# Kernel tuning notes

Hardware: AMD Instinct MI355X
Metric: run time of the kernel (lower is better)

Reference implementation:

```python
import jax, jax.numpy as jnp
import numpy as np
import math

H, KV, D, HID, WIN = 8, 4, 256, 2048, 1024  # heads, kv heads, head_dim, hidden, sliding window
B, S = 1, 2048

def _rms(x, scale):
    # Gemma3RMSNorm: hardcoded 1e-6 eps, (1+scale) gain
    var = jnp.mean(jnp.square(x), axis=-1, keepdims=True)
    return x * jax.lax.rsqrt(var + 1e-6) * (1.0 + scale)

def _rot_half(x):
    x1, x2 = jnp.split(x, 2, axis=-1)
    return jnp.concatenate((-x2, x1), axis=-1)

def setup_inputs() -> dict:
    key = jax.random.key(0)
    ks = jax.random.split(key, 8)
    x = jax.random.normal(ks[0], (B, S, HID), jnp.float32)
    attn_mask = jnp.ones((B, S), jnp.bool_)
    segment_pos = jnp.broadcast_to(jnp.arange(S, dtype=jnp.int32)[None], (B, S))
    # true RoPE tables, theta=1e6 (Gemma3 global layers)
    inv_freq = 1.0 / (1e6 ** (np.arange(0, D, 2, dtype=np.float32) / D))
    ang = np.arange(S, dtype=np.float32)[:, None] * inv_freq[None, :]  # [S, D/2]
    emb = np.concatenate([ang, ang], axis=-1)                          # [S, D]
    cos = jnp.asarray(np.cos(emb), jnp.float32)[None]                  # [1, S, D]
    sin = jnp.asarray(np.sin(emb), jnp.float32)[None]
    sd = 1.0 / math.sqrt(HID)
    wq = jax.random.normal(ks[1], (HID, H * D), jnp.float32) * sd
    wk = jax.random.normal(ks[2], (HID, KV * D), jnp.float32) * sd
    wv = jax.random.normal(ks[3], (HID, KV * D), jnp.float32) * sd
    wo = jax.random.normal(ks[4], (H * D, HID), jnp.float32) * (1.0 / math.sqrt(H * D))
    q_scale = jnp.zeros((D,), jnp.float32)  # zeros_init as in module
    k_scale = jnp.zeros((D,), jnp.float32)
    return dict(x=x, attn_mask=attn_mask, segment_pos=segment_pos, cos=cos, sin=sin,
                wq=wq, wk=wk, wv=wv, wo=wo, q_scale=q_scale, k_scale=k_scale)

def reference(x, attn_mask, segment_pos, cos, sin, wq, wk, wv, wo, q_scale, k_scale):
    b, s, _ = x.shape
    # projections -> [b, h, s, d]
    q = (x @ wq).reshape(b, s, H, D).transpose(0, 2, 1, 3)
    k = (x @ wk).reshape(b, s, KV, D).transpose(0, 2, 1, 3)
    v = (x @ wv).reshape(b, s, KV, D).transpose(0, 2, 1, 3)
    # per-head QK RMSNorm
    q = _rms(q, q_scale)
    k = _rms(k, k_scale)
    # RoPE (cos/sin broadcast over head axis, unsqueeze_dim=1)
    c, sn = cos[:, None], sin[:, None]
    q = q * c + _rot_half(q) * sn
    k = k * c + _rot_half(k) * sn
    # GQA: repeat-interleave kv heads
    rep = H // KV
    k = jnp.repeat(k, rep, axis=1)
    v = jnp.repeat(v, rep, axis=1)
    scores = jnp.einsum('bhqd,bhkd->bhqk', q, k) / math.sqrt(D)
    # causal + padding mask (q_len > 1 path, no image bidirectional mask)
    causal = jnp.tril(jnp.ones((s, s), jnp.bool_))
    mask = causal[None] & attn_mask[:, None, :]          # [b, q, kv]
    # sliding window mask (prefill: cache positions = arange)
    kvpos = jnp.arange(s)
    pos = segment_pos[:, :, None]
    sliding = (kvpos[None, None] > pos - WIN) & (kvpos[None, None] < pos + WIN)
    full = mask & sliding
    scores = scores + jnp.where(full[:, None], 0.0, -1e37)
    w = jax.nn.softmax(scores.astype(jnp.float32), axis=-1).astype(scores.dtype)
    out = jnp.einsum('bhqk,bhkd->bhqd', w, v)
    out = out.transpose(0, 2, 1, 3).reshape(b, s, H * D)
    return out @ wo
```

## Files before the change

### kernel.cpp

```cpp
#include <hip/hip_runtime.h>
#include <hip/hip_bf16.h>

#define S_LEN 2048
#define HID 2048
#define NH 8
#define NKV 4
#define HD 256
#define WIN 1024

typedef __hip_bfloat16 bf16;
typedef __attribute__((ext_vector_type(8))) short bf16x8;
typedef __attribute__((ext_vector_type(4))) float f32x4;

__device__ __forceinline__ void gld_lds16(void* lds, const void* g) {
    __builtin_amdgcn_global_load_lds(
        (const __attribute__((address_space(1))) unsigned int*)g,
        (__attribute__((address_space(3))) unsigned int*)lds,
        16, 0, 0);
}


__global__ __launch_bounds__(256)
void conv_f32_bf16(const float* __restrict__ s, bf16* __restrict__ d, int n8) {
    const int i = blockIdx.x * 256 + threadIdx.x;
    if (i >= n8) return;
    float4 a = ((const float4*)s)[i * 2];
    float4 b = ((const float4*)s)[i * 2 + 1];
    union { uint4 v; bf16 h[8]; } u;
    u.h[0] = __float2bfloat16(a.x); u.h[1] = __float2bfloat16(a.y);
    u.h[2] = __float2bfloat16(a.z); u.h[3] = __float2bfloat16(a.w);
    u.h[4] = __float2bfloat16(b.x); u.h[5] = __float2bfloat16(b.y);
    u.h[6] = __float2bfloat16(b.z); u.h[7] = __float2bfloat16(b.w);
    ((uint4*)d)[i] = u.v;
}

__global__ __launch_bounds__(256)
void convT_f32_bf16(const float* __restrict__ src, bf16* __restrict__ dst, int R, int C) {
    __shared__ bf16 Ts[64][72];
    const int tid = threadIdx.x;
    const int r0 = blockIdx.y * 64, c0 = blockIdx.x * 64;
    {
        const int r = tid >> 2;
        const int cq = (tid & 3) * 16;
#pragma unroll
        for (int j = 0; j < 16; j += 4) {
            float4 v = *(const float4*)&src[(size_t)(r0 + r) * C + c0 + cq + j];
            Ts[cq + j + 0][r] = __float2bfloat16(v.x);
            Ts[cq + j + 1][r] = __float2bfloat16(v.y);
            Ts[cq + j + 2][r] = __float2bfloat16(v.z);
            Ts[cq + j + 3][r] = __float2bfloat16(v.w);
        }
    }
    __syncthreads();
    {
        const int c = tid >> 2;
        const int rq = (tid & 3) * 16;
#pragma unroll
        for (int j = 0; j < 16; j += 8)
            *(uint4*)&dst[(size_t)(c0 + c) * R + r0 + rq + j] = *(const uint4*)&Ts[c][rq + j];
    }
}

template<int MODE>
__global__ __launch_bounds__(256)
void gemm_mfma2(const bf16* __restrict__ A, const bf16* __restrict__ Bt,
                float* __restrict__ C, bf16* __restrict__ Qo,
                bf16* __restrict__ Ko, bf16* __restrict__ Vto,
                int N, int K) {
    __shared__ bf16 As[128][32];
    __shared__ bf16 Bs[64][32];
    const int tid = threadIdx.x;
    const int w = tid >> 6, lane = tid & 63;
    const int lnm = lane & 15, quad = lane >> 4;
    const int wm = (w & 1) * 64, wn = (w >> 1) * 32;
    const int m0 = blockIdx.y * 128, n0 = blockIdx.x * 64;

    const int lr = lane >> 2;
    const int lc = (lane & 3) * 8;

    f32x4 acc[4][2];
#pragma unroll
    for (int i = 0; i < 4; ++i)
#pragma unroll
        for (int j = 0; j < 2; ++j) acc[i][j] = (f32x4){0.f, 0.f, 0.f, 0.f};

    const bf16* a0 = A + (size_t)(m0 + 32 * w + lr) * K + lc;
    const bf16* a1 = A + (size_t)(m0 + 32 * w + 16 + lr) * K + lc;
    const bf16* b0 = Bt + (size_t)(n0 + 16 * w + lr) * K + lc;

    for (int k0 = 0; k0 < K; k0 += 32) {
        gld_lds16(&As[32 * w][0],      a0 + k0);
        gld_lds16(&As[32 * w + 16][0], a1 + k0);
        gld_lds16(&Bs[16 * w][0],      b0 + k0);
        __syncthreads();
        bf16x8 af[4], bfr[2];
#pragma unroll
        for (int t = 0; t < 4; ++t) af[t] = *(const bf16x8*)&As[wm + t * 16 + lnm][quad * 8];
#pragma unroll
        for (int t = 0; t < 2; ++t) bfr[t] = *(const bf16x8*)&Bs[wn + t * 16 + lnm][quad * 8];
#pragma unroll
        for (int tm = 0; tm < 4; ++tm)
#pragma unroll
            for (int tn = 0; tn < 2; ++tn)
                acc[tm][tn] = __builtin_amdgcn_mfma_f32_16x16x32_bf16(
                    af[tm], bfr[tn], acc[tm][tn], 0, 0, 0);
        __syncthreads();
    }

#pragma unroll
    for (int tm = 0; tm < 4; ++tm)
#pragma unroll
        for (int tn = 0; tn < 2; ++tn)
#pragma unroll
            for (int r = 0; r < 4; ++r) {
                const int row = m0 + wm + tm * 16 + quad * 4 + r;
                const int col = n0 + wn + tn * 16 + lnm;
                const float v = acc[tm][tn][r];
                if constexpr (MODE == 0) {
                    C[(size_t)row * N + col] = v;
                } else {
                    if (col < 2048)
                        Qo[(size_t)row * (NH * HD) + col] = __float2bfloat16(v);
                    else if (col < 3072)
                        Ko[(size_t)row * (NKV * HD) + col - 2048] = __float2bfloat16(v);
                    else
                        Vto[(size_t)(col - 3072) * S_LEN + row] = __float2bfloat16(v);
                }
            }
}

__global__ __launch_bounds__(64)
void rmsrope_kernel(bf16* __restrict__ Q, bf16* __restrict__ Kb,
                    const float* __restrict__ cosb, const float* __restrict__ sinb,
                    const float* __restrict__ qscale, const float* __restrict__ kscale,
                    float qmul) {
    const int p = blockIdx.x;
    const int hg = blockIdx.y;
    const int lane = threadIdx.x;

    bf16* base;
    const float* scale;
    float mul;
    if (hg < NH) { base = Q + (size_t)p * (NH * HD) + hg * HD; scale = qscale; mul = qmul; }
    else         { base = Kb + (size_t)p * (NKV * HD) + (hg - NH) * HD; scale = kscale; mul = 1.f; }

    const int d0 = lane * 2;
    float x0 = (float)base[d0],       x1 = (float)base[d0 + 1];
    float y0 = (float)base[d0 + 128], y1 = (float)base[d0 + 129];

    float ss = x0 * x0 + x1 * x1 + y0 * y0 + y1 * y1;
#pragma unroll
    for (int off = 32; off > 0; off >>= 1) ss += __shfl_xor(ss, off, 64);
    const float r = rsqrtf(ss * (1.0f / (float)HD) + 1e-6f);

    x0 *= r * (1.f + scale[d0]);
    x1 *= r * (1.f + scale[d0 + 1]);
    y0 *= r * (1.f + scale[d0 + 128]);
    y1 *= r * (1.f + scale[d0 + 129]);

    const size_t cb = (size_t)p * HD;
    const float c0 = cosb[cb + d0],       c1 = cosb[cb + d0 + 1];
    const float cA = cosb[cb + d0 + 128], cB = cosb[cb + d0 + 129];
    const float s0 = sinb[cb + d0],       s1 = sinb[cb + d0 + 1];
    const float sA = sinb[cb + d0 + 128], sB = sinb[cb + d0 + 129];

    base[d0]       = __float2bfloat16((x0 * c0 - y0 * s0) * mul);
    base[d0 + 1]   = __float2bfloat16((x1 * c1 - y1 * s1) * mul);
    base[d0 + 128] = __float2bfloat16((y0 * cA + x0 * sA) * mul);
    base[d0 + 129] = __float2bfloat16((y1 * cB + x1 * sB) * mul);
}

__global__ __launch_bounds__(256)
void attn_mfma(const bf16* __restrict__ Q, const bf16* __restrict__ K,
               const bf16* __restrict__ Vt, bf16* __restrict__ Op,
               float2* __restrict__ ml) {
    __shared__ bf16 Ks[32][264];
    __shared__ bf16 Vs[256][40];
    __shared__ bf16 Pl[4][16][40];
    const int qt = blockIdx.x, h = blockIdx.y, chunk = blockIdx.z, kvh = h >> 1;
    const int tid = threadIdx.x, w = tid >> 6, lane = tid & 63;
    const int lnm = lane & 15, quad = lane >> 4;

    bf16x8 qf[8];
    const int qrow = qt * 64 + w * 16 + lnm;
#pragma unroll
    for (int s = 0; s < 8; ++s)
        qf[s] = *(const bf16x8*)&Q[(size_t)qrow * HID + h * HD + s * 32 + quad * 8];

    f32x4 o[16];
#pragma unroll
    for (int i = 0; i < 16; ++i) o[i] = (f32x4){0.f, 0.f, 0.f, 0.f};
    float M[4] = {-3e38f, -3e38f, -3e38f, -3e38f};
    float L[4] = {0.f, 0.f, 0.f, 0.f};

    const int ktlo = (qt >= 16) ? (2 * qt - 32) : 0;
    const int kthi = 2 * qt + 1;
    const int ntile = kthi - ktlo + 1;
    const int half = (ntile + 1) >> 1;
    const int c0 = ktlo + (chunk ? half : 0);
    const int c1 = chunk ? kthi : (ktlo + half - 1);

    for (int kt = c0; kt <= c1; ++kt) {
#pragma unroll
        for (int p = 0; p < 4; ++p) {
            const int row = p * 8 + (tid >> 5);
            const int d8 = (tid & 31) * 8;
            *(uint4*)&Ks[row][d8] =
                *(const uint4*)&K[(size_t)(kt * 32 + row) * (NKV * HD) + kvh * HD + d8];
        }
#pragma unroll
        for (int p = 0; p < 4; ++p) {
            const int d = p * 64 + (tid >> 2);
            const int c8 = (tid & 3) * 8;
            *(uint4*)&Vs[d][c8] =
                *(const uint4*)&Vt[(size_t)(kvh * HD + d) * S_LEN + kt * 32 + c8];
        }
        __syncthreads();

        f32x4 s4[2];
        s4[0] = (f32x4){0.f, 0.f, 0.f, 0.f};
        s4[1] = (f32x4){0.f, 0.f, 0.f, 0.f};
#pragma unroll
        for (int t = 0; t < 2; ++t)
#pragma unroll
            for (int s = 0; s < 8; ++s) {
                bf16x8 kf = *(const bf16x8*)&Ks[t * 16 + lnm][s * 32 + quad * 8];
                s4[t] = __builtin_amdgcn_mfma_f32_16x16x32_bf16(qf[s], kf, s4[t], 0, 0, 0);
            }
#pragma unroll
        for (int t = 0; t < 2; ++t)
#pragma unroll
            for (int r = 0; r < 4; ++r) {
                const int m_g = qt * 64 + w * 16 + quad * 4 + r;
                const int n_g = kt * 32 + t * 16 + lnm;
                if (n_g > m_g || n_g + (WIN - 1) < m_g) s4[t][r] = -1e30f;
            }
        float mx[4], rs[4], al[4];
#pragma unroll
        for (int r = 0; r < 4; ++r) {
            mx[r] = fmaxf(s4[0][r], s4[1][r]);
#pragma unroll
            for (int off = 1; off < 16; off <<= 1)
                mx[r] = fmaxf(mx[r], __shfl_xor(mx[r], off, 64));
            const float Mn = fmaxf(M[r], mx[r]);
            al[r] = __expf(M[r] - Mn);
            M[r] = Mn;
        }
#pragma unroll
        for (int t = 0; t < 2; ++t)
#pragma unroll
            for (int r = 0; r < 4; ++r)
                s4[t][r] = __expf(s4[t][r] - M[r]);
#pragma unroll
        for (int r = 0; r < 4; ++r) {
            rs[r] = s4[0][r] + s4[1][r];
#pragma unroll
            for (int off = 1; off < 16; off <<= 1)
                rs[r] += __shfl_xor(rs[r], off, 64);
            L[r] = L[r] * al[r] + rs[r];
        }
#pragma unroll
        for (int t2 = 0; t2 < 16; ++t2)
#pragma unroll
            for (int r = 0; r < 4; ++r) o[t2][r] *= al[r];
#pragma unroll
        for (int t = 0; t < 2; ++t)
#pragma unroll
            for (int r = 0; r < 4; ++r)
                Pl[w][quad * 4 + r][t * 16 + lnm] = __float2bfloat16(s4[t][r]);
        bf16x8 pa = *(const bf16x8*)&Pl[w][lnm][quad * 8];
#pragma unroll
        for (int t2 = 0; t2 < 16; ++t2) {
            bf16x8 vb = *(const bf16x8*)&Vs[t2 * 16 + lnm][quad * 8];
            o[t2] = __builtin_amdgcn_mfma_f32_16x16x32_bf16(pa, vb, o[t2], 0, 0, 0);
        }
        __syncthreads();
    }

    float rL[4];
#pragma unroll
    for (int r = 0; r < 4; ++r) rL[r] = 1.f / L[r];
    bf16* Opc = Op + (size_t)chunk * S_LEN * HID;
#pragma unroll
    for (int t2 = 0; t2 < 16; ++t2)
#pragma unroll
        for (int r = 0; r < 4; ++r)
            Opc[(size_t)(qt * 64 + w * 16 + quad * 4 + r) * HID + h * HD + t2 * 16 + lnm] =
                __float2bfloat16(o[t2][r] * rL[r]);
    if (lnm == 0) {
#pragma unroll
        for (int r = 0; r < 4; ++r) {
            const int row = qt * 64 + w * 16 + quad * 4 + r;
            ml[((size_t)chunk * S_LEN + row) * NH + h] = make_float2(M[r], L[r]);
        }
    }
}

__global__ __launch_bounds__(256)
void attn_combine(const bf16* __restrict__ Op, const float2* __restrict__ ml,
                  bf16* __restrict__ O) {
    const int row = blockIdx.x, h = blockIdx.y, d = threadIdx.x;
    const float2 a = ml[(size_t)row * NH + h];
    const float2 b = ml[((size_t)S_LEN + row) * NH + h];
    const float Mx = fmaxf(a.x, b.x);
    const float wa = a.y * __expf(a.x - Mx);
    const float wb = b.y * __expf(b.x - Mx);
    const float inv = 1.0f / (wa + wb);
    const size_t idx = (size_t)row * HID + h * HD + d;
    const float oa = (float)Op[idx];
    const float ob = (float)Op[(size_t)S_LEN * HID + idx];
    O[idx] = __float2bfloat16((wa * oa + wb * ob) * inv);
}

extern "C" void kernel_launch(void* const* d_in, const int* in_sizes, int n_in,
                              void* d_out, int out_size, void* d_ws, size_t ws_size,
                              hipStream_t stream) {
    const float* xf   = (const float*)d_in[0];
    const float* cosb = (const float*)d_in[3];
    const float* sinb = (const float*)d_in[4];
    const float* wqf  = (const float*)d_in[5];
    const float* wkf  = (const float*)d_in[6];
    const float* wvf  = (const float*)d_in[7];
    const float* wof  = (const float*)d_in[8];
    const float* qs   = (const float*)d_in[9];
    const float* ks   = (const float*)d_in[10];
    float* out = (float*)d_out;
    char* ws = (char*)d_ws;

    bf16*   wqkvt = (bf16*)(ws);
    bf16*   Op    = (bf16*)(ws);
    bf16*   wot   = (bf16*)(ws + (16ull << 20));
    bf16*   xb    = (bf16*)(ws + (24ull << 20));
    bf16*   Ab    = (bf16*)(ws + (24ull << 20));
    bf16*   Qb    = (bf16*)(ws + (32ull << 20));
    bf16*   Kb    = (bf16*)(ws + (40ull << 20));
    bf16*   Vtb   = (bf16*)(ws + (44ull << 20));
    float2* ml    = (float2*)(ws + (48ull << 20));

    dim3 blk(256);

    conv_f32_bf16<<<2048, blk, 0, stream>>>(xf, xb, (S_LEN * HID) / 8);
    convT_f32_bf16<<<dim3(32, 32), blk, 0, stream>>>(wqf, wqkvt, HID, NH * HD);
    convT_f32_bf16<<<dim3(16, 32), blk, 0, stream>>>(wkf, wqkvt + (size_t)2048 * HID, HID, NKV * HD);
    convT_f32_bf16<<<dim3(16, 32), blk, 0, stream>>>(wvf, wqkvt + (size_t)3072 * HID, HID, NKV * HD);
    convT_f32_bf16<<<dim3(32, 32), blk, 0, stream>>>(wof, wot, NH * HD, HID);

    gemm_mfma2<1><<<dim3(64, 16), blk, 0, stream>>>(xb, wqkvt, nullptr, Qb, Kb, Vtb, 4096, HID);

    rmsrope_kernel<<<dim3(S_LEN, NH + NKV), dim3(64), 0, stream>>>(
        Qb, Kb, cosb, sinb, qs, ks, 0.0625f);

    attn_mfma<<<dim3(S_LEN / 64, NH, 2), blk, 0, stream>>>(Qb, Kb, Vtb, Op, ml);
    attn_combine<<<dim3(S_LEN, NH), blk, 0, stream>>>(Op, ml, Ab);

    gemm_mfma2<0><<<dim3(32, 16), blk, 0, stream>>>(Ab, wot, out, nullptr, nullptr, nullptr, HID, HID);
}
```

Baseline: 309.2 us.

## Widen QKV GEMM tile, use fragment-ordered LDS layout, and fuse QKV weight transposes

The GEMM is rewritten so each lane's global-to-LDS load lands directly in MFMA fragment order. Fragment reads from LDS then become contiguous per-lane 16-byte loads, which should cut bank conflicts and address math. The QKV projection moves to a 128-wide N tile, halving the block count and improving A-tile reuse, at the cost of more accumulator registers per wave. The three separate Q/K/V weight transpose launches are merged into one kernel to save launch overhead.

```diff
diff --git a/kernel.cpp b/kernel.cpp
--- a/kernel.cpp
+++ b/kernel.cpp
@@ -34,11 +34,10 @@
     ((uint4*)d)[i] = u.v;
 }
 
-__global__ __launch_bounds__(256)
-void convT_f32_bf16(const float* __restrict__ src, bf16* __restrict__ dst, int R, int C) {
+__device__ __forceinline__ void transT_body(const float* __restrict__ src, bf16* __restrict__ dst,
+                                            int R, int C, int r0, int c0) {
     __shared__ bf16 Ts[64][72];
     const int tid = threadIdx.x;
-    const int r0 = blockIdx.y * 64, c0 = blockIdx.x * 64;
     {
         const int r = tid >> 2;
         const int cq = (tid & 3) * 16;
@@ -61,47 +60,84 @@
     }
 }
 
-template<int MODE>
-__global__ __launch_bounds__(256)
-void gemm_mfma2(const bf16* __restrict__ A, const bf16* __restrict__ Bt,
+__global__ __launch_bounds__(256)
+void convT_f32_bf16(const float* __restrict__ src, bf16* __restrict__ dst, int R, int C) {
+    transT_body(src, dst, R, C, blockIdx.y * 64, blockIdx.x * 64);
+}
+
+__global__ __launch_bounds__(256)
+void convT_qkv(const float* __restrict__ wq, const float* __restrict__ wk,
+               const float* __restrict__ wv, bf16* __restrict__ dst) {
+    const int bx = blockIdx.x;
+    const float* src; int C, c0, drow0;
+    if (bx < 32)      { src = wq; C = 2048; c0 = bx * 64;        drow0 = bx * 64; }
+    else if (bx < 48) { src = wk; C = 1024; c0 = (bx - 32) * 64; drow0 = 2048 + (bx - 32) * 64; }
+    else              { src = wv; C = 1024; c0 = (bx - 48) * 64; drow0 = 3072 + (bx - 48) * 64; }
+    bf16* dshift = dst + ((size_t)drow0 - c0) * HID;
+    transT_body(src, dshift, HID, C, blockIdx.y * 64, c0);
+}
+
+template<int BN_T, int MODE>
+__global__ __launch_bounds__(256)
+void gemm_mfma3(const bf16* __restrict__ A, const bf16* __restrict__ Bt,
                 float* __restrict__ C, bf16* __restrict__ Qo,
                 bf16* __restrict__ Ko, bf16* __restrict__ Vto,
                 int N, int K) {
-    __shared__ bf16 As[128][32];
-    __shared__ bf16 Bs[64][32];
+    constexpr int NBF = BN_T / 32;
+    __shared__ bf16 As[8 * 512];
+    __shared__ bf16 Bs[(BN_T / 16) * 512];
     const int tid = threadIdx.x;
     const int w = tid >> 6, lane = tid & 63;
     const int lnm = lane & 15, quad = lane >> 4;
-    const int wm = (w & 1) * 64, wn = (w >> 1) * 32;
-    const int m0 = blockIdx.y * 128, n0 = blockIdx.x * 64;
-
-    const int lr = lane >> 2;
-    const int lc = (lane & 3) * 8;
-
-    f32x4 acc[4][2];
+    const int wm = (w & 1) * 64, wn = (w >> 1) * (BN_T / 2);
+    const int m0 = blockIdx.y * 128, n0 = blockIdx.x * BN_T;
+
+    const int srow = lane & 15;
+    const int skc  = lane >> 4;
+
+    f32x4 acc[4][NBF];
 #pragma unroll
     for (int i = 0; i < 4; ++i)
 #pragma unroll
-        for (int j = 0; j < 2; ++j) acc[i][j] = (f32x4){0.f, 0.f, 0.f, 0.f};
-
-    const bf16* a0 = A + (size_t)(m0 + 32 * w + lr) * K + lc;
-    const bf16* a1 = A + (size_t)(m0 + 32 * w + 16 + lr) * K + lc;
-    const bf16* b0 = Bt + (size_t)(n0 + 16 * w + lr) * K + lc;
+        for (int j = 0; j < NBF; ++j) acc[i][j] = (f32x4){0.f, 0.f, 0.f, 0.f};
+
+    const bf16* ga0 = A + (size_t)(m0 + 32 * w + srow) * K + skc * 8;
+    const bf16* ga1 = ga0 + (size_t)16 * K;
+    const bf16* gb0;
+    const bf16* gb1 = nullptr;
+    if constexpr (BN_T == 128) {
+        gb0 = Bt + (size_t)(n0 + 32 * w + srow) * K + skc * 8;
+        gb1 = gb0 + (size_t)16 * K;
+    } else {
+        gb0 = Bt + (size_t)(n0 + 16 * w + srow) * K + skc * 8;
+    }
+
+    const int ca = wm >> 4;
+    const int cb = wn >> 4;
 
     for (int k0 = 0; k0 < K; k0 += 32) {
-        gld_lds16(&As[32 * w][0],      a0 + k0);
-        gld_lds16(&As[32 * w + 16][0], a1 + k0);
-        gld_lds16(&Bs[16 * w][0],      b0 + k0);
+        gld_lds16(&As[(2 * w) * 512],     ga0 + k0);
+        gld_lds16(&As[(2 * w + 1) * 512], ga1 + k0);
+        if constexpr (BN_T == 128) {
+            gld_lds16(&Bs[(2 * w) * 512],     gb0 + k0);
+            gld_lds16(&Bs[(2 * w + 1) * 512], gb1 + k0);
+        } else {
+            gld_lds16(&Bs[w * 512], gb0 + k0);
+        }
         __syncthreads();
-        bf16x8 af[4], bfr[2];
-#pragma unroll
-        for (int t = 0; t < 4; ++t) af[t] = *(const bf16x8*)&As[wm + t * 16 + lnm][quad * 8];
-#pragma unroll
-        for (int t = 0; t < 2; ++t) bfr[t] = *(const bf16x8*)&Bs[wn + t * 16 + lnm][quad * 8];
+
+        bf16x8 af[4], bfr[NBF];
+#pragma unroll
+        for (int t = 0; t < 4; ++t)
+            af[t] = *(const bf16x8*)&As[(ca + t) * 512 + lane * 8];
+#pragma unroll
+        for (int t = 0; t < NBF; ++t)
+            bfr[t] = *(const bf16x8*)&Bs[(cb + t) * 512 + lane * 8];
+
 #pragma unroll
         for (int tm = 0; tm < 4; ++tm)
 #pragma unroll
-            for (int tn = 0; tn < 2; ++tn)
+            for (int tn = 0; tn < NBF; ++tn)
                 acc[tm][tn] = __builtin_amdgcn_mfma_f32_16x16x32_bf16(
                     af[tm], bfr[tn], acc[tm][tn], 0, 0, 0);
         __syncthreads();
@@ -110,7 +146,7 @@
 #pragma unroll
     for (int tm = 0; tm < 4; ++tm)
 #pragma unroll
-        for (int tn = 0; tn < 2; ++tn)
+        for (int tn = 0; tn < NBF; ++tn)
 #pragma unroll
             for (int r = 0; r < 4; ++r) {
                 const int row = m0 + wm + tm * 16 + quad * 4 + r;
@@ -340,12 +376,11 @@
     dim3 blk(256);
 
     conv_f32_bf16<<<2048, blk, 0, stream>>>(xf, xb, (S_LEN * HID) / 8);
-    convT_f32_bf16<<<dim3(32, 32), blk, 0, stream>>>(wqf, wqkvt, HID, NH * HD);
-    convT_f32_bf16<<<dim3(16, 32), blk, 0, stream>>>(wkf, wqkvt + (size_t)2048 * HID, HID, NKV * HD);
-    convT_f32_bf16<<<dim3(16, 32), blk, 0, stream>>>(wvf, wqkvt + (size_t)3072 * HID, HID, NKV * HD);
+    convT_qkv<<<dim3(64, 32), blk, 0, stream>>>(wqf, wkf, wvf, wqkvt);
     convT_f32_bf16<<<dim3(32, 32), blk, 0, stream>>>(wof, wot, NH * HD, HID);
 
-    gemm_mfma2<1><<<dim3(64, 16), blk, 0, stream>>>(xb, wqkvt, nullptr, Qb, Kb, Vtb, 4096, HID);
+    gemm_mfma3<128, 1><<<dim3(32, 16), blk, 0, stream>>>(
+        xb, wqkvt, nullptr, Qb, Kb, Vtb, 4096, HID);
 
     rmsrope_kernel<<<dim3(S_LEN, NH + NKV), dim3(64), 0, stream>>>(
         Qb, Kb, cosb, sinb, qs, ks, 0.0625f);
@@ -353,5 +388,6 @@
     attn_mfma<<<dim3(S_LEN / 64, NH, 2), blk, 0, stream>>>(Qb, Kb, Vtb, Op, ml);
     attn_combine<<<dim3(S_LEN, NH), blk, 0, stream>>>(Op, ml, Ab);
 
-    gemm_mfma2<0><<<dim3(32, 16), blk, 0, stream>>>(Ab, wot, out, nullptr, nullptr, nullptr, HID, HID);
-}
+    gemm_mfma3<64, 0><<<dim3(32, 16), blk, 0, stream>>>(
+        Ab, wot, out, nullptr, nullptr, nullptr, HID, HID);
+}
```

Result: slower. 334.7 us (+8.3%).
